# Kernel optimization log

Measured on AMD Instinct MI355X. Metric: run time of the kernel, lower is better.

## Reference

```python
import jax, jax.numpy as jnp
import numpy as np

R, C = 9, 9  # local window (rows, cols)


def setup_inputs() -> dict:
    key = jax.random.key(0)
    k1, k2, k3, k4, k5 = jax.random.split(key, 5)
    q = jax.random.normal(k1, (8, 256, 128, 128), jnp.float32)      # (B, q_size, H, W)
    c_t = jax.random.normal(k2, (8, 256, 512), jnp.float32)          # (B, T, c_size)
    W_a = jax.random.normal(k3, (512, 256), jnp.float32) * 0.04      # Linear(q_size -> c_size), no bias
    W_p = jax.random.normal(k4, (256, 512), jnp.float32) * 0.04      # Linear(c_size -> p_size)
    V_p = jax.random.normal(k5, (2, 256), jnp.float32) * 0.06        # Linear(p_size -> 2)
    return {"q": q, "c_t": c_t, "W_a": W_a, "W_p": W_p, "V_p": V_p}


def reference(q, c_t, W_a, W_p, V_p):
    B, D, H, W = q.shape
    T = c_t.shape[1]
    S = H  # q.size(2) before padding

    # predictive alignment: p_t = S * sigmoid(V_p(tanh(W_p(c_t))))  -> (B, T, 2)
    p_t = S * jax.nn.sigmoid(jnp.tanh(c_t @ W_p.T) @ V_p.T)

    # pad top/left with NaN, flatten spatial dims
    qp = jnp.pad(q, ((0, 0), (0, 0), (1, 0), (1, 0)), constant_values=jnp.nan)
    rows, cols = H + 1, W + 1
    qf = qp.reshape(B, D, rows * cols).transpose(0, 2, 1)  # (B, rows*cols, D)

    roff = jnp.arange(-(R // 2), (R + 1) // 2)  # R offsets
    coff = jnp.arange(-(C // 2), (C + 1) // 2)  # C offsets
    r = jnp.clip(jnp.round(p_t[..., 0]).astype(jnp.int32)[..., None] + roff + 1, 0, rows) % rows  # (B,T,R)
    c = jnp.clip(jnp.round(p_t[..., 1]).astype(jnp.int32)[..., None] + coff + 1, 0, cols) % cols  # (B,T,C)

    # flat window indices, order i*C + j (matches torch stack order)
    s = (r[..., :, None] * cols + c[..., None, :]).reshape(B, T, R * C)

    # gather windows: (B, T, R*C, D)
    qg = jnp.take_along_axis(qf, s.reshape(B, T * R * C, 1), axis=1).reshape(B, T, R * C, D)
    nan_loc = jnp.isnan(qg[..., 0])                    # (B, T, R*C)
    qg = jnp.where(nan_loc[..., None], 0.0, qg)

    # Gaussian positional weighting
    rexp = -2.0 * ((jnp.clip(r - 1, 0, None).astype(jnp.float32) - p_t[..., 0:1]) / (R // 2)) ** 2
    cexp = -2.0 * ((jnp.clip(c - 1, 0, None).astype(jnp.float32) - p_t[..., 1:2]) / (C // 2)) ** 2
    gauss = jnp.exp((rexp[..., :, None] + cexp[..., None, :]).reshape(B, T, R * C))

    # score: (W_a q) . c_t  -> (B, T, R*C)
    a_t = jnp.einsum('btkd,cd,btc->btk', qg, W_a, c_t)
    a_t = jnp.where(nan_loc, -jnp.inf, a_t)
    W_attn = jax.nn.softmax(a_t, axis=2) * gauss

    out = jnp.einsum('btk,btkd->btd', W_attn, qg)  # (B, T, D)
    return out
```

## Files before the change

kernel.cpp:

```cpp
#include <hip/hip_runtime.h>
#include <math.h>

#define Bq 8
#define Tt 256
#define Dd 256
#define Hh 128
#define Ww 128
#define Cc 512
#define HW (Hh*Ww)
#define NBT (Bq*Tt)

__device__ __forceinline__ float lane_bcast(float x, int l) {
    return __uint_as_float(__builtin_amdgcn_readlane(__float_as_uint(x), l));
}

__global__ __launch_bounds__(256) void transpose_wp(
    const float* __restrict__ W_p, float* __restrict__ WpT)
{
    __shared__ float tile[32][33];
    const int bx = blockIdx.x;
    const int by = blockIdx.y;
    const int lx = threadIdx.x & 31, ly = threadIdx.x >> 5;
#pragma unroll
    for (int j = 0; j < 4; j++) {
        int p = by * 32 + ly + j * 8;
        tile[ly + j * 8][lx] = W_p[(size_t)p * Cc + bx * 32 + lx];
    }
    __syncthreads();
#pragma unroll
    for (int j = 0; j < 4; j++) {
        int c = bx * 32 + ly + j * 8;
        WpT[(size_t)c * 256 + by * 32 + lx] = tile[lx][ly + j * 8];
    }
}

#define TOK 8
__global__ __launch_bounds__(512) void prep_kernel(
    const float* __restrict__ c_t,
    const float* __restrict__ W_a,
    const float* __restrict__ WpT,
    const float* __restrict__ V_p,
    float* __restrict__ u_ws,
    float* __restrict__ p_ws)
{
    __shared__ float y0s[TOK][256];
    __shared__ float y1s[TOK][256];
    const int tid  = threadIdx.x;
    const int o    = tid & 255;
    const int half = tid >> 8;
    const int ln   = tid & 63;
    const int bt0  = blockIdx.x * TOK;

    const float* Wcol = (half ? WpT : W_a) + o;
    const float* ctb  = c_t + (size_t)bt0 * Cc;

    float acc[TOK];
#pragma unroll
    for (int t = 0; t < TOK; t++) acc[t] = 0.f;

    float ctr[TOK], ctn[TOK];
#pragma unroll
    for (int t = 0; t < TOK; t++) ctr[t] = ctb[t * Cc + ln];

#pragma unroll
    for (int c0 = 0; c0 < Cc; c0 += 64) {
        if (c0 + 64 < Cc) {
#pragma unroll
            for (int t = 0; t < TOK; t++) ctn[t] = ctb[t * Cc + c0 + 64 + ln];
        }
#pragma unroll
        for (int cc8 = 0; cc8 < 64; cc8 += 8) {
            float w[8];
#pragma unroll
            for (int j = 0; j < 8; j++)
                w[j] = Wcol[(size_t)(c0 + cc8 + j) * 256];
#pragma unroll
            for (int j = 0; j < 8; j++) {
#pragma unroll
                for (int t = 0; t < TOK; t++)
                    acc[t] = fmaf(lane_bcast(ctr[t], cc8 + j), w[j], acc[t]);
            }
        }
#pragma unroll
        for (int t = 0; t < TOK; t++) ctr[t] = ctn[t];
    }

    if (half == 0) {
#pragma unroll
        for (int t = 0; t < TOK; t++)
            u_ws[(size_t)(bt0 + t) * Dd + o] = acc[t];
    } else {
        float v0 = V_p[o], v1 = V_p[256 + o];
#pragma unroll
        for (int t = 0; t < TOK; t++) {
            float th = tanhf(acc[t]);
            y0s[t][o] = th * v0;
            y1s[t][o] = th * v1;
        }
    }
    __syncthreads();

    const int wv = tid >> 6;
    float s0 = y0s[wv][ln] + y0s[wv][ln + 64] + y0s[wv][ln + 128] + y0s[wv][ln + 192];
    float s1 = y1s[wv][ln] + y1s[wv][ln + 64] + y1s[wv][ln + 128] + y1s[wv][ln + 192];
#pragma unroll
    for (int of = 32; of >= 1; of >>= 1) {
        s0 += __shfl_xor(s0, of);
        s1 += __shfl_xor(s1, of);
    }
    if (ln == 0) {
        p_ws[(size_t)(bt0 + wv) * 2 + 0] = 128.f / (1.f + expf(-s0));
        p_ws[(size_t)(bt0 + wv) * 2 + 1] = 128.f / (1.f + expf(-s1));
    }
}

__global__ __launch_bounds__(512, 4) void attn_kernel(
    const float* __restrict__ q,
    const float* __restrict__ u_ws,
    const float* __restrict__ p_ws,
    float* __restrict__ out)
{
    __shared__ __align__(16) _Float16 win[Dd][9][12];
    __shared__ __align__(16) float pacc_s[16][9][12];
    __shared__ float ascore[9][12];
    __shared__ float u_s[Dd];
    __shared__ float w_s[81];
    __shared__ float a_s[81];
    __shared__ float e_s[81];
    __shared__ float rex_s[9], cex_s[9];
    __shared__ int   rr_s[9], cc_s[9];
    __shared__ float m_sh, inv_sh;

    const int tid = threadIdx.x;
    int bt = blockIdx.x;
    bt = ((bt & 7) << 8) | (bt >> 3);
    const int b = bt >> 8;

    if (tid < Dd) u_s[tid] = u_ws[(size_t)bt * Dd + tid];

    if (tid < 18) {
        int   i = (tid < 9) ? tid : tid - 9;
        float p = p_ws[(size_t)bt * 2 + ((tid < 9) ? 0 : 1)];
        int base = (int)rintf(p);
        int v = base + i - 3;
        v = min(max(v, 0), 129) % 129;
        float cl = (float)max(v - 1, 0);
        float z  = (cl - p) * 0.25f;
        float ex = -2.f * z * z;
        if (tid < 9) { rr_s[i] = v; rex_s[i] = ex; }
        else         { cc_s[i] = v; cex_s[i] = ex; }
    }
    __syncthreads();

    int jc0 = 0, c0 = 1;
#pragma unroll
    for (int j = 8; j >= 0; j--)
        if (cc_s[j] > 0) { jc0 = j; c0 = cc_s[j]; }
    const int cb = min((c0 - 1) & ~3, Ww - 12);
    const int e0 = (c0 - 1) - cb;

    {
        const int g  = tid >> 5;
        const int l5 = tid & 31;
        const bool lact = (l5 < 27);
        const int li = lact ? ((l5 * 171) >> 9) : 0;
        const int lv = l5 - li * 3;
        const int vr = lact ? rr_s[li] : 1;
        const int rowoff = (max(vr, 1) - 1) * Ww + cb + 4 * lv;
        const float* qp = q + (size_t)b * Dd * HW + rowoff;

        if (lact) {
            float u_r[16];
#pragma unroll
            for (int m = 0; m < 16; m++) u_r[m] = u_s[g + 16 * m];

            float px = 0.f, py = 0.f, pz = 0.f, pw = 0.f;
            float4 xb[2][4];
#pragma unroll
            for (int mm = 0; mm < 4; mm++)
                xb[0][mm] = *(const float4*)(qp + (size_t)(g + 16 * mm) * HW);

            for (int it = 0; it < 4; it++) {
                const int cur = it & 1;
                if (it < 3) {
#pragma unroll
                    for (int mm = 0; mm < 4; mm++)
                        xb[cur ^ 1][mm] = *(const float4*)
                            (qp + (size_t)(g + 16 * (4 * (it + 1) + mm)) * HW);
                }
#pragma unroll
                for (int mm = 0; mm < 4; mm++) {
                    const int m  = 4 * it + mm;
                    const int d0 = g + 16 * m;
                    float4 x = xb[cur][mm];
                    float  u = u_r[m];
                    px = fmaf(x.x, u, px); py = fmaf(x.y, u, py);
                    pz = fmaf(x.z, u, pz); pw = fmaf(x.w, u, pw);
                    union { _Float16 h[4]; uint2 uu; } pk;
                    pk.h[0] = (_Float16)x.x; pk.h[1] = (_Float16)x.y;
                    pk.h[2] = (_Float16)x.z; pk.h[3] = (_Float16)x.w;
                    *(uint2*)&win[d0][li][4 * lv] = pk.uu;
                }
            }
            *(float4*)&pacc_s[g][li][4 * lv] = make_float4(px, py, pz, pw);
        }
    }
    __syncthreads();

    if (tid < 108) {
        const int li  = tid / 12;
        const int pos = tid - li * 12;
        float s = 0.f;
#pragma unroll
        for (int g = 0; g < 16; g++) s += pacc_s[g][li][pos];
        ascore[li][pos] = s;
    }
    __syncthreads();

    float a_val = -INFINITY;
    bool  valid_k = false;
    if (tid < 81) {
        const int ki = (tid * 57) >> 9;
        const int kj = tid - ki * 9;
        valid_k = (rr_s[ki] > 0) && (cc_s[kj] > 0);
        const int pos = min(max(e0 + kj - jc0, 0), 11);
        a_val = valid_k ? ascore[ki][pos] : -INFINITY;
        a_s[tid] = a_val;
    }
    __syncthreads();

    if (tid < 64) {
        float m = a_s[tid];
        if (tid + 64 < 81) m = fmaxf(m, a_s[tid + 64]);
        for (int o = 32; o >= 1; o >>= 1) m = fmaxf(m, __shfl_xor(m, o));
        if (tid == 0) m_sh = m;
    }
    __syncthreads();
    {
        float e = 0.f;
        if (tid < 81 && valid_k) e = expf(a_val - m_sh);
        if (tid < 81) e_s[tid] = e;
    }
    __syncthreads();
    if (tid < 64) {
        float sv = e_s[tid] + ((tid + 64 < 81) ? e_s[tid + 64] : 0.f);
        for (int o = 32; o >= 1; o >>= 1) sv += __shfl_xor(sv, o);
        if (tid == 0) inv_sh = 1.f / sv;
    }
    __syncthreads();
    if (tid < 81) {
        int i = (tid * 57) >> 9;
        int j = tid - i * 9;
        float g = expf(rex_s[i] + cex_s[j]);
        w_s[tid] = e_s[tid] * inv_sh * g;
    }
    __syncthreads();

    float* pacc2 = &pacc_s[0][0][0];
    {
        const int h  = tid >> 8;
        const int dd = tid & 255;
        int posj[9];
#pragma unroll
        for (int j = 0; j < 9; j++) posj[j] = min(max(e0 + j - jc0, 0), 11);
        const _Float16* wd = &win[dd][0][0];
        float acc = 0.f;
        if (h == 0) {
#pragma unroll
            for (int k = 0; k < 41; k++) {
                const int ki = k / 9, kj = k % 9;
                acc = fmaf(w_s[k], (float)wd[ki * 12 + posj[kj]], acc);
            }
        } else {
#pragma unroll
            for (int k = 41; k < 81; k++) {
                const int ki = k / 9, kj = k % 9;
                acc = fmaf(w_s[k], (float)wd[ki * 12 + posj[kj]], acc);
            }
        }
        pacc2[h * 256 + dd] = acc;
    }
    __syncthreads();
    if (tid < Dd) out[(size_t)bt * Dd + tid] = pacc2[tid] + pacc2[256 + tid];
}

extern "C" void kernel_launch(void* const* d_in, const int* in_sizes, int n_in,
                              void* d_out, int out_size, void* d_ws, size_t ws_size,
                              hipStream_t stream) {
    const float* q   = (const float*)d_in[0];
    const float* c_t = (const float*)d_in[1];
    const float* W_a = (const float*)d_in[2];
    const float* W_p = (const float*)d_in[3];
    const float* V_p = (const float*)d_in[4];
    float* out  = (float*)d_out;
    float* u_ws = (float*)d_ws;
    float* p_ws = u_ws + (size_t)NBT * Dd;
    float* WpT  = p_ws + (size_t)NBT * 2;

    transpose_wp<<<dim3(16, 8), 256, 0, stream>>>(W_p, WpT);
    prep_kernel<<<NBT / TOK, 512, 0, stream>>>(c_t, W_a, WpT, V_p, u_ws, p_ws);
    attn_kernel<<<NBT, 512, 0, stream>>>(q, u_ws, p_ws, out);
}
```

Measured before the change: 263.9 us.

## Sort tokens by window position per batch to improve cache locality

Adds a per-batch bitonic sort kernel that orders the tokens by their rounded window centre (row, col). The attention kernel then processes tokens in this sorted order, so consecutive blocks gather overlapping windows of q and get more L2/MALL reuse. This costs one extra small kernel launch and an indirection load per block.

```diff
diff --git a/kernel.cpp b/kernel.cpp
--- a/kernel.cpp
+++ b/kernel.cpp
@@ -114,10 +114,36 @@
     }
 }
 
+__global__ __launch_bounds__(256) void order_kernel(
+    const float* __restrict__ p_ws, int* __restrict__ order)
+{
+    __shared__ unsigned kv[256];
+    const int b = blockIdx.x, t = threadIdx.x;
+    const float p0 = p_ws[(size_t)(b * 256 + t) * 2 + 0];
+    const float p1 = p_ws[(size_t)(b * 256 + t) * 2 + 1];
+    const int r = min(max((int)rintf(p0), 0), 129);
+    const int c = min(max((int)rintf(p1), 0), 129);
+    kv[t] = (((unsigned)(r * 130 + c)) << 8) | (unsigned)t;
+    __syncthreads();
+    for (int k = 2; k <= 256; k <<= 1) {
+        for (int j = k >> 1; j >= 1; j >>= 1) {
+            const int ixj = t ^ j;
+            if (ixj > t) {
+                const unsigned a = kv[t], bb = kv[ixj];
+                const bool up = ((t & k) == 0);
+                if (up ? (a > bb) : (a < bb)) { kv[t] = bb; kv[ixj] = a; }
+            }
+            __syncthreads();
+        }
+    }
+    order[b * 256 + t] = (int)(kv[t] & 0xFFu);
+}
+
 __global__ __launch_bounds__(512, 4) void attn_kernel(
     const float* __restrict__ q,
     const float* __restrict__ u_ws,
     const float* __restrict__ p_ws,
+    const int*   __restrict__ order,
     float* __restrict__ out)
 {
     __shared__ __align__(16) _Float16 win[Dd][9][12];
@@ -135,12 +161,13 @@
     int bt = blockIdx.x;
     bt = ((bt & 7) << 8) | (bt >> 3);
     const int b = bt >> 8;
-
-    if (tid < Dd) u_s[tid] = u_ws[(size_t)bt * Dd + tid];
+    const int tok = (b << 8) | order[bt];
+
+    if (tid < Dd) u_s[tid] = u_ws[(size_t)tok * Dd + tid];
 
     if (tid < 18) {
         int   i = (tid < 9) ? tid : tid - 9;
-        float p = p_ws[(size_t)bt * 2 + ((tid < 9) ? 0 : 1)];
+        float p = p_ws[(size_t)tok * 2 + ((tid < 9) ? 0 : 1)];
         int base = (int)rintf(p);
         int v = base + i - 3;
         v = min(max(v, 0), 129) % 129;
@@ -281,7 +308,7 @@
         pacc2[h * 256 + dd] = acc;
     }
     __syncthreads();
-    if (tid < Dd) out[(size_t)bt * Dd + tid] = pacc2[tid] + pacc2[256 + tid];
+    if (tid < Dd) out[(size_t)tok * Dd + tid] = pacc2[tid] + pacc2[256 + tid];
 }
 
 extern "C" void kernel_launch(void* const* d_in, const int* in_sizes, int n_in,
@@ -296,8 +323,10 @@
     float* u_ws = (float*)d_ws;
     float* p_ws = u_ws + (size_t)NBT * Dd;
     float* WpT  = p_ws + (size_t)NBT * 2;
+    int*   ord  = (int*)(WpT + (size_t)Cc * 256);
 
     transpose_wp<<<dim3(16, 8), 256, 0, stream>>>(W_p, WpT);
     prep_kernel<<<NBT / TOK, 512, 0, stream>>>(c_t, W_a, WpT, V_p, u_ws, p_ws);
-    attn_kernel<<<NBT, 512, 0, stream>>>(q, u_ws, p_ws, out);
-}
+    order_kernel<<<Bq, 256, 0, stream>>>(p_ws, ord);
+    attn_kernel<<<NBT, 512, 0, stream>>>(q, u_ws, p_ws, ord, out);
+}
```

Result: slower. 270.5 us (+2.5%).

## Fuse projection prep into attention kernel with per-block token loop and window prefetch

Applied to the files above, without the earlier changes.

Merges the prep kernel (W_a projection and predictive-alignment position) into the attention kernel. Each block now computes u and p for 8 tokens into shared memory, then loops over those tokens, prefetching the next token's q window into registers while the current token's softmax and weighted sum run. This removes the workspace round trip for u and p and one kernel launch. In exchange the grid shrinks from 2048 blocks to 256, so each CU has far fewer resident waves and the tokens in a block run one after another.

```diff
diff --git a/kernel.cpp b/kernel.cpp
--- a/kernel.cpp
+++ b/kernel.cpp
@@ -9,6 +9,7 @@
 #define Cc 512
 #define HW (Hh*Ww)
 #define NBT (Bq*Tt)
+#define TOK 8
 
 __device__ __forceinline__ float lane_bcast(float x, int l) {
     return __uint_as_float(__builtin_amdgcn_readlane(__float_as_uint(x), l));
@@ -34,254 +35,259 @@
     }
 }
 
-#define TOK 8
-__global__ __launch_bounds__(512) void prep_kernel(
+__global__ __launch_bounds__(512, 2) void fused_kernel(
+    const float* __restrict__ q,
     const float* __restrict__ c_t,
     const float* __restrict__ W_a,
     const float* __restrict__ WpT,
     const float* __restrict__ V_p,
-    float* __restrict__ u_ws,
-    float* __restrict__ p_ws)
-{
-    __shared__ float y0s[TOK][256];
-    __shared__ float y1s[TOK][256];
-    const int tid  = threadIdx.x;
-    const int o    = tid & 255;
-    const int half = tid >> 8;
-    const int ln   = tid & 63;
-    const int bt0  = blockIdx.x * TOK;
-
-    const float* Wcol = (half ? WpT : W_a) + o;
-    const float* ctb  = c_t + (size_t)bt0 * Cc;
-
-    float acc[TOK];
-#pragma unroll
-    for (int t = 0; t < TOK; t++) acc[t] = 0.f;
-
-    float ctr[TOK], ctn[TOK];
-#pragma unroll
-    for (int t = 0; t < TOK; t++) ctr[t] = ctb[t * Cc + ln];
-
-#pragma unroll
-    for (int c0 = 0; c0 < Cc; c0 += 64) {
-        if (c0 + 64 < Cc) {
-#pragma unroll
-            for (int t = 0; t < TOK; t++) ctn[t] = ctb[t * Cc + c0 + 64 + ln];
-        }
-#pragma unroll
-        for (int cc8 = 0; cc8 < 64; cc8 += 8) {
-            float w[8];
-#pragma unroll
-            for (int j = 0; j < 8; j++)
-                w[j] = Wcol[(size_t)(c0 + cc8 + j) * 256];
-#pragma unroll
-            for (int j = 0; j < 8; j++) {
-#pragma unroll
-                for (int t = 0; t < TOK; t++)
-                    acc[t] = fmaf(lane_bcast(ctr[t], cc8 + j), w[j], acc[t]);
-            }
-        }
-#pragma unroll
-        for (int t = 0; t < TOK; t++) ctr[t] = ctn[t];
-    }
-
-    if (half == 0) {
-#pragma unroll
-        for (int t = 0; t < TOK; t++)
-            u_ws[(size_t)(bt0 + t) * Dd + o] = acc[t];
-    } else {
-        float v0 = V_p[o], v1 = V_p[256 + o];
-#pragma unroll
-        for (int t = 0; t < TOK; t++) {
-            float th = tanhf(acc[t]);
-            y0s[t][o] = th * v0;
-            y1s[t][o] = th * v1;
-        }
-    }
-    __syncthreads();
-
-    const int wv = tid >> 6;
-    float s0 = y0s[wv][ln] + y0s[wv][ln + 64] + y0s[wv][ln + 128] + y0s[wv][ln + 192];
-    float s1 = y1s[wv][ln] + y1s[wv][ln + 64] + y1s[wv][ln + 128] + y1s[wv][ln + 192];
-#pragma unroll
-    for (int of = 32; of >= 1; of >>= 1) {
-        s0 += __shfl_xor(s0, of);
-        s1 += __shfl_xor(s1, of);
-    }
-    if (ln == 0) {
-        p_ws[(size_t)(bt0 + wv) * 2 + 0] = 128.f / (1.f + expf(-s0));
-        p_ws[(size_t)(bt0 + wv) * 2 + 1] = 128.f / (1.f + expf(-s1));
-    }
-}
-
-__global__ __launch_bounds__(512, 4) void attn_kernel(
-    const float* __restrict__ q,
-    const float* __restrict__ u_ws,
-    const float* __restrict__ p_ws,
     float* __restrict__ out)
 {
-    __shared__ __align__(16) _Float16 win[Dd][9][12];
+    __shared__ __align__(16) unsigned char win_raw[55296];
+    __shared__ __align__(16) float u8s[TOK][256];
     __shared__ __align__(16) float pacc_s[16][9][12];
     __shared__ float ascore[9][12];
-    __shared__ float u_s[Dd];
     __shared__ float w_s[81];
     __shared__ float a_s[81];
     __shared__ float e_s[81];
     __shared__ float rex_s[9], cex_s[9];
     __shared__ int   rr_s[9], cc_s[9];
     __shared__ float m_sh, inv_sh;
+    __shared__ float p8[TOK][2];
+
+    _Float16 (*win)[9][12] = (_Float16(*)[9][12])win_raw;
+    float (*y0s)[256] = (float(*)[256])win_raw;
+    float (*y1s)[256] = (float(*)[256])(win_raw + 8192);
 
     const int tid = threadIdx.x;
-    int bt = blockIdx.x;
-    bt = ((bt & 7) << 8) | (bt >> 3);
-    const int b = bt >> 8;
-
-    if (tid < Dd) u_s[tid] = u_ws[(size_t)bt * Dd + tid];
-
-    if (tid < 18) {
-        int   i = (tid < 9) ? tid : tid - 9;
-        float p = p_ws[(size_t)bt * 2 + ((tid < 9) ? 0 : 1)];
-        int base = (int)rintf(p);
-        int v = base + i - 3;
-        v = min(max(v, 0), 129) % 129;
-        float cl = (float)max(v - 1, 0);
-        float z  = (cl - p) * 0.25f;
-        float ex = -2.f * z * z;
-        if (tid < 9) { rr_s[i] = v; rex_s[i] = ex; }
-        else         { cc_s[i] = v; cex_s[i] = ex; }
+    const int bid = blockIdx.x;
+    const int b   = bid & 7;
+    const int bt0 = b * 256 + (bid >> 3) * TOK;
+
+    {
+        const int o    = tid & 255;
+        const int half = tid >> 8;
+        const int ln   = tid & 63;
+        const float* Wcol = (half ? WpT : W_a) + o;
+        const float* ctb  = c_t + (size_t)bt0 * Cc;
+
+        float acc[TOK];
+#pragma unroll
+        for (int t = 0; t < TOK; t++) acc[t] = 0.f;
+
+        float ctr[TOK], ctn[TOK];
+#pragma unroll
+        for (int t = 0; t < TOK; t++) ctr[t] = ctb[t * Cc + ln];
+
+#pragma unroll
+        for (int c0 = 0; c0 < Cc; c0 += 64) {
+            if (c0 + 64 < Cc) {
+#pragma unroll
+                for (int t = 0; t < TOK; t++) ctn[t] = ctb[t * Cc + c0 + 64 + ln];
+            }
+#pragma unroll
+            for (int cc8 = 0; cc8 < 64; cc8 += 8) {
+                float w[8];
+#pragma unroll
+                for (int j = 0; j < 8; j++)
+                    w[j] = Wcol[(size_t)(c0 + cc8 + j) * 256];
+#pragma unroll
+                for (int j = 0; j < 8; j++) {
+#pragma unroll
+                    for (int t = 0; t < TOK; t++)
+                        acc[t] = fmaf(lane_bcast(ctr[t], cc8 + j), w[j], acc[t]);
+                }
+            }
+#pragma unroll
+            for (int t = 0; t < TOK; t++) ctr[t] = ctn[t];
+        }
+
+        if (half == 0) {
+#pragma unroll
+            for (int t = 0; t < TOK; t++)
+                u8s[t][o] = acc[t];
+        } else {
+            float v0 = V_p[o], v1 = V_p[256 + o];
+#pragma unroll
+            for (int t = 0; t < TOK; t++) {
+                float th = tanhf(acc[t]);
+                y0s[t][o] = th * v0;
+                y1s[t][o] = th * v1;
+            }
+        }
+        __syncthreads();
+
+        const int wv = tid >> 6;
+        float s0 = y0s[wv][ln] + y0s[wv][ln + 64] + y0s[wv][ln + 128] + y0s[wv][ln + 192];
+        float s1 = y1s[wv][ln] + y1s[wv][ln + 64] + y1s[wv][ln + 128] + y1s[wv][ln + 192];
+#pragma unroll
+        for (int of = 32; of >= 1; of >>= 1) {
+            s0 += __shfl_xor(s0, of);
+            s1 += __shfl_xor(s1, of);
+        }
+        if (ln == 0) {
+            p8[wv][0] = 128.f / (1.f + expf(-s0));
+            p8[wv][1] = 128.f / (1.f + expf(-s1));
+        }
     }
     __syncthreads();
 
-    int jc0 = 0, c0 = 1;
-#pragma unroll
-    for (int j = 8; j >= 0; j--)
-        if (cc_s[j] > 0) { jc0 = j; c0 = cc_s[j]; }
-    const int cb = min((c0 - 1) & ~3, Ww - 12);
-    const int e0 = (c0 - 1) - cb;
-
-    {
-        const int g  = tid >> 5;
-        const int l5 = tid & 31;
-        const bool lact = (l5 < 27);
-        const int li = lact ? ((l5 * 171) >> 9) : 0;
-        const int lv = l5 - li * 3;
-        const int vr = lact ? rr_s[li] : 1;
-        const int rowoff = (max(vr, 1) - 1) * Ww + cb + 4 * lv;
-        const float* qp = q + (size_t)b * Dd * HW + rowoff;
+    const int g  = tid >> 5;
+    const int l5 = tid & 31;
+    const bool lact = (l5 < 27);
+    const int li = lact ? ((l5 * 171) >> 9) : 0;
+    const int lv = l5 - li * 3;
+    const float* qb = q + (size_t)b * Dd * HW;
+
+    float4 xb[16];
+
+    if (lact) {
+        const float p0 = p8[0][0], p1 = p8[0][1];
+        const int b0 = (int)rintf(p0);
+        const int vv = min(max(b0 + li - 3, 0), 129) % 129;
+        const int row = max(vv, 1) - 1;
+        const int b1 = (int)rintf(p1);
+        const int c0n = max(b1 - 3, 1);
+        const int cbn = min((c0n - 1) & ~3, Ww - 12);
+        const float* qp = qb + row * Ww + cbn + 4 * lv;
+#pragma unroll
+        for (int m = 0; m < 16; m++)
+            xb[m] = *(const float4*)(qp + (size_t)(g + 16 * m) * HW);
+    }
+
+    for (int t = 0; t < TOK; ++t) {
+        const int tok = bt0 + t;
+        if (tid < 18) {
+            int   i = (tid < 9) ? tid : tid - 9;
+            float p = p8[t][(tid < 9) ? 0 : 1];
+            int base = (int)rintf(p);
+            int v = min(max(base + i - 3, 0), 129) % 129;
+            float cl = (float)max(v - 1, 0);
+            float z  = (cl - p) * 0.25f;
+            float ex = -2.f * z * z;
+            if (tid < 9) { rr_s[i] = v; rex_s[i] = ex; }
+            else         { cc_s[i] = v; cex_s[i] = ex; }
+        }
+        __syncthreads();
+
+        int jc0 = 0, c0 = 1;
+#pragma unroll
+        for (int j = 8; j >= 0; j--)
+            if (cc_s[j] > 0) { jc0 = j; c0 = cc_s[j]; }
+        const int cb = min((c0 - 1) & ~3, Ww - 12);
+        const int e0 = (c0 - 1) - cb;
 
         if (lact) {
             float u_r[16];
 #pragma unroll
-            for (int m = 0; m < 16; m++) u_r[m] = u_s[g + 16 * m];
-
+            for (int m = 0; m < 16; m++) u_r[m] = u8s[t][g + 16 * m];
             float px = 0.f, py = 0.f, pz = 0.f, pw = 0.f;
-            float4 xb[2][4];
-#pragma unroll
-            for (int mm = 0; mm < 4; mm++)
-                xb[0][mm] = *(const float4*)(qp + (size_t)(g + 16 * mm) * HW);
-
-            for (int it = 0; it < 4; it++) {
-                const int cur = it & 1;
-                if (it < 3) {
-#pragma unroll
-                    for (int mm = 0; mm < 4; mm++)
-                        xb[cur ^ 1][mm] = *(const float4*)
-                            (qp + (size_t)(g + 16 * (4 * (it + 1) + mm)) * HW);
+#pragma unroll
+            for (int m = 0; m < 16; m++) {
+                const float4 x = xb[m];
+                const float  u = u_r[m];
+                px = fmaf(x.x, u, px); py = fmaf(x.y, u, py);
+                pz = fmaf(x.z, u, pz); pw = fmaf(x.w, u, pw);
+                union { _Float16 h[4]; uint2 uu; } pk;
+                pk.h[0] = (_Float16)x.x; pk.h[1] = (_Float16)x.y;
+                pk.h[2] = (_Float16)x.z; pk.h[3] = (_Float16)x.w;
+                *(uint2*)&win[g + 16 * m][li][4 * lv] = pk.uu;
+            }
+            *(float4*)&pacc_s[g][li][4 * lv] = make_float4(px, py, pz, pw);
+        }
+        __syncthreads();
+
+        if (tid < 108) {
+            const int lii = tid / 12;
+            const int pos = tid - lii * 12;
+            float s = 0.f;
+#pragma unroll
+            for (int gg = 0; gg < 16; gg++) s += pacc_s[gg][lii][pos];
+            ascore[lii][pos] = s;
+        }
+        __syncthreads();
+
+        float a_val = -INFINITY;
+        bool  valid_k = false;
+        if (tid < 81) {
+            const int ki = (tid * 57) >> 9;
+            const int kj = tid - ki * 9;
+            valid_k = (rr_s[ki] > 0) && (cc_s[kj] > 0);
+            const int pos = min(max(e0 + kj - jc0, 0), 11);
+            a_val = valid_k ? ascore[ki][pos] : -INFINITY;
+            a_s[tid] = a_val;
+        }
+        __syncthreads();
+
+        if (tid < 64) {
+            float m = a_s[tid];
+            if (tid + 64 < 81) m = fmaxf(m, a_s[tid + 64]);
+            for (int o = 32; o >= 1; o >>= 1) m = fmaxf(m, __shfl_xor(m, o));
+            if (tid == 0) m_sh = m;
+        }
+        __syncthreads();
+        {
+            float e = 0.f;
+            if (tid < 81 && valid_k) e = expf(a_val - m_sh);
+            if (tid < 81) e_s[tid] = e;
+        }
+        __syncthreads();
+        if (tid < 64) {
+            float sv = e_s[tid] + ((tid + 64 < 81) ? e_s[tid + 64] : 0.f);
+            for (int o = 32; o >= 1; o >>= 1) sv += __shfl_xor(sv, o);
+            if (tid == 0) inv_sh = 1.f / sv;
+        }
+        __syncthreads();
+        if (tid < 81) {
+            int i = (tid * 57) >> 9;
+            int j = tid - i * 9;
+            float gw = expf(rex_s[i] + cex_s[j]);
+            w_s[tid] = e_s[tid] * inv_sh * gw;
+        }
+        __syncthreads();
+
+        if (t + 1 < TOK && lact) {
+            const float p0 = p8[t + 1][0], p1 = p8[t + 1][1];
+            const int b0 = (int)rintf(p0);
+            const int vv = min(max(b0 + li - 3, 0), 129) % 129;
+            const int row = max(vv, 1) - 1;
+            const int b1 = (int)rintf(p1);
+            const int c0n = max(b1 - 3, 1);
+            const int cbn = min((c0n - 1) & ~3, Ww - 12);
+            const float* qp = qb + row * Ww + cbn + 4 * lv;
+#pragma unroll
+            for (int m = 0; m < 16; m++)
+                xb[m] = *(const float4*)(qp + (size_t)(g + 16 * m) * HW);
+        }
+
+        float* pacc2 = &pacc_s[0][0][0];
+        {
+            const int h  = tid >> 8;
+            const int dd = tid & 255;
+            int posj[9];
+#pragma unroll
+            for (int j = 0; j < 9; j++) posj[j] = min(max(e0 + j - jc0, 0), 11);
+            const _Float16* wd = &win[dd][0][0];
+            float acc = 0.f;
+            if (h == 0) {
+#pragma unroll
+                for (int k = 0; k < 41; k++) {
+                    const int ki = k / 9, kj = k % 9;
+                    acc = fmaf(w_s[k], (float)wd[ki * 12 + posj[kj]], acc);
                 }
-#pragma unroll
-                for (int mm = 0; mm < 4; mm++) {
-                    const int m  = 4 * it + mm;
-                    const int d0 = g + 16 * m;
-                    float4 x = xb[cur][mm];
-                    float  u = u_r[m];
-                    px = fmaf(x.x, u, px); py = fmaf(x.y, u, py);
-                    pz = fmaf(x.z, u, pz); pw = fmaf(x.w, u, pw);
-                    union { _Float16 h[4]; uint2 uu; } pk;
-                    pk.h[0] = (_Float16)x.x; pk.h[1] = (_Float16)x.y;
-                    pk.h[2] = (_Float16)x.z; pk.h[3] = (_Float16)x.w;
-                    *(uint2*)&win[d0][li][4 * lv] = pk.uu;
+            } else {
+#pragma unroll
+                for (int k = 41; k < 81; k++) {
+                    const int ki = k / 9, kj = k % 9;
+                    acc = fmaf(w_s[k], (float)wd[ki * 12 + posj[kj]], acc);
                 }
             }
-            *(float4*)&pacc_s[g][li][4 * lv] = make_float4(px, py, pz, pw);
-        }
-    }
-    __syncthreads();
-
-    if (tid < 108) {
-        const int li  = tid / 12;
-        const int pos = tid - li * 12;
-        float s = 0.f;
-#pragma unroll
-        for (int g = 0; g < 16; g++) s += pacc_s[g][li][pos];
-        ascore[li][pos] = s;
-    }
-    __syncthreads();
-
-    float a_val = -INFINITY;
-    bool  valid_k = false;
-    if (tid < 81) {
-        const int ki = (tid * 57) >> 9;
-        const int kj = tid - ki * 9;
-        valid_k = (rr_s[ki] > 0) && (cc_s[kj] > 0);
-        const int pos = min(max(e0 + kj - jc0, 0), 11);
-        a_val = valid_k ? ascore[ki][pos] : -INFINITY;
-        a_s[tid] = a_val;
-    }
-    __syncthreads();
-
-    if (tid < 64) {
-        float m = a_s[tid];
-        if (tid + 64 < 81) m = fmaxf(m, a_s[tid + 64]);
-        for (int o = 32; o >= 1; o >>= 1) m = fmaxf(m, __shfl_xor(m, o));
-        if (tid == 0) m_sh = m;
-    }
-    __syncthreads();
-    {
-        float e = 0.f;
-        if (tid < 81 && valid_k) e = expf(a_val - m_sh);
-        if (tid < 81) e_s[tid] = e;
-    }
-    __syncthreads();
-    if (tid < 64) {
-        float sv = e_s[tid] + ((tid + 64 < 81) ? e_s[tid + 64] : 0.f);
-        for (int o = 32; o >= 1; o >>= 1) sv += __shfl_xor(sv, o);
-        if (tid == 0) inv_sh = 1.f / sv;
-    }
-    __syncthreads();
-    if (tid < 81) {
-        int i = (tid * 57) >> 9;
-        int j = tid - i * 9;
-        float g = expf(rex_s[i] + cex_s[j]);
-        w_s[tid] = e_s[tid] * inv_sh * g;
-    }
-    __syncthreads();
-
-    float* pacc2 = &pacc_s[0][0][0];
-    {
-        const int h  = tid >> 8;
-        const int dd = tid & 255;
-        int posj[9];
-#pragma unroll
-        for (int j = 0; j < 9; j++) posj[j] = min(max(e0 + j - jc0, 0), 11);
-        const _Float16* wd = &win[dd][0][0];
-        float acc = 0.f;
-        if (h == 0) {
-#pragma unroll
-            for (int k = 0; k < 41; k++) {
-                const int ki = k / 9, kj = k % 9;
-                acc = fmaf(w_s[k], (float)wd[ki * 12 + posj[kj]], acc);
-            }
-        } else {
-#pragma unroll
-            for (int k = 41; k < 81; k++) {
-                const int ki = k / 9, kj = k % 9;
-                acc = fmaf(w_s[k], (float)wd[ki * 12 + posj[kj]], acc);
-            }
-        }
-        pacc2[h * 256 + dd] = acc;
-    }
-    __syncthreads();
-    if (tid < Dd) out[(size_t)bt * Dd + tid] = pacc2[tid] + pacc2[256 + tid];
+            pacc2[h * 256 + dd] = acc;
+        }
+        __syncthreads();
+        if (tid < Dd) out[(size_t)tok * Dd + tid] = pacc2[tid] + pacc2[256 + tid];
+        __syncthreads();
+    }
 }
 
 extern "C" void kernel_launch(void* const* d_in, const int* in_sizes, int n_in,
@@ -293,11 +299,8 @@
     const float* W_p = (const float*)d_in[3];
     const float* V_p = (const float*)d_in[4];
     float* out  = (float*)d_out;
-    float* u_ws = (float*)d_ws;
-    float* p_ws = u_ws + (size_t)NBT * Dd;
-    float* WpT  = p_ws + (size_t)NBT * 2;
+    float* WpT  = (float*)d_ws;
 
     transpose_wp<<<dim3(16, 8), 256, 0, stream>>>(W_p, WpT);
-    prep_kernel<<<NBT / TOK, 512, 0, stream>>>(c_t, W_a, WpT, V_p, u_ws, p_ws);
-    attn_kernel<<<NBT, 512, 0, stream>>>(q, u_ws, p_ws, out);
+    fused_kernel<<<NBT / TOK, 512, 0, stream>>>(q, c_t, W_a, WpT, V_p, out);
 }
```

After: 272.8 us. 1.03x slower.
